# Performance work log

Hardware: AMD Instinct MI355X
Metric: run time of the kernel (lower is better)

Reference implementation:

```python
import jax, jax.numpy as jnp
import numpy as np

B, S, E = 2, 2048, 2048
H, KV, HD = 16, 4, 128          # attn heads, kv heads, head_dim = E//H
GROUPS = H // KV
I = 8192                        # intermediate_size
EPS = 1e-6
ROPE_THETA = 10000.0
SCALE = HD ** -0.5


def _rope_tables(seq_len, head_dim, dtype=jnp.float32):
    inv_freq = 1.0 / (ROPE_THETA ** (jnp.arange(0, head_dim, 2, dtype=jnp.float32) / head_dim))
    pos = jnp.arange(seq_len, dtype=jnp.float32)
    ang = pos[:, None] * inv_freq[None, :]            # [S, HD/2]
    emb = jnp.concatenate([ang, ang], axis=-1)        # [S, HD]
    return jnp.cos(emb).astype(dtype), jnp.sin(emb).astype(dtype)


def _rotate_half(x):
    x1, x2 = jnp.split(x, 2, axis=-1)
    return jnp.concatenate([-x2, x1], axis=-1)


def _apply_rope(x, cos, sin):
    # x: [B, h, S, HD]; cos/sin: [S, HD]
    return x * cos[None, None] + _rotate_half(x) * sin[None, None]


def _rmsnorm(x, w, eps=EPS):
    var = jnp.mean(jnp.square(x), axis=-1, keepdims=True)
    return x * jax.lax.rsqrt(var + eps) * w


def setup_inputs() -> dict:
    key = jax.random.key(0)
    ks = jax.random.split(key, 12)
    sd = lambda fan_in: 1.0 / np.sqrt(fan_in)
    inp = {
        "x": jax.random.normal(ks[0], (B, S, E), dtype=jnp.float32),
        "attn_mask": jnp.zeros((B, 1, S, S), dtype=jnp.bool_),
        "wq": jax.random.normal(ks[1], (E, E), dtype=jnp.float32) * sd(E),
        "bq": jnp.zeros((E,), dtype=jnp.float32),
        "wkv": jax.random.normal(ks[2], (2 * KV * HD, E), dtype=jnp.float32) * sd(E),
        "bkv": jnp.zeros((2 * KV * HD,), dtype=jnp.float32),
        "wo": jax.random.normal(ks[3], (E, E), dtype=jnp.float32) * sd(E),
        "w_gate": jax.random.normal(ks[4], (I, E), dtype=jnp.float32) * sd(E),
        "w_up": jax.random.normal(ks[5], (I, E), dtype=jnp.float32) * sd(E),
        "w_down": jax.random.normal(ks[6], (E, I), dtype=jnp.float32) * sd(I),
        "norm1_w": jnp.ones((E,), dtype=jnp.float32),
        "norm2_w": jnp.ones((E,), dtype=jnp.float32),
    }
    return inp


def reference(x, attn_mask, wq, bq, wkv, bkv, wo, w_gate, w_up, w_down, norm1_w, norm2_w):
    # ---- attention block ----
    y = _rmsnorm(x, norm1_w)
    q = y @ wq.T + bq                                     # [B,S,E]
    kv = y @ wkv.T + bkv                                  # [B,S,2*KV*HD]
    k, v = jnp.split(kv, 2, axis=-1)
    q = q.reshape(B, S, H, HD).transpose(0, 2, 1, 3)      # [B,H,S,HD]
    k = k.reshape(B, S, KV, HD).transpose(0, 2, 1, 3)     # [B,KV,S,HD]
    v = v.reshape(B, S, KV, HD).transpose(0, 2, 1, 3)
    cos, sin = _rope_tables(S, HD, dtype=q.dtype)
    q = _apply_rope(q, cos, sin)
    k = _apply_rope(k, cos, sin)
    # GQA expand kv heads
    k = jnp.repeat(k, GROUPS, axis=1)                     # [B,H,S,HD]
    v = jnp.repeat(v, GROUPS, axis=1)
    # NOTE: source Qwen2Attention.forward never applies attn_mask — faithful here.
    scores = jnp.einsum('bhsd,bhtd->bhst', q, k) * SCALE  # [B,H,S,S]
    attn = jax.nn.softmax(scores, axis=-1)
    o = jnp.einsum('bhst,bhtd->bhsd', attn, v)            # [B,H,S,HD]
    o = o.transpose(0, 2, 1, 3).reshape(B, S, E) @ wo.T
    x = x + o
    # ---- MLP block (SwiGLU) ----
    y = _rmsnorm(x, norm2_w)
    h = jax.nn.silu(y @ w_gate.T) * (y @ w_up.T)          # [B,S,I]
    x = x + h @ w_down.T
    return x
```

## Files before the change

kernel.cpp:

```cpp
#include <hip/hip_runtime.h>

typedef __bf16 bf16;
typedef __bf16 bf16x8 __attribute__((ext_vector_type(8)));
typedef __bf16 bf16x4 __attribute__((ext_vector_type(4)));
typedef float f32x4 __attribute__((ext_vector_type(4)));

#define DEV __device__ __forceinline__

constexpr int B_ = 2, S_ = 2048, E_ = 2048, H_ = 16, KVH_ = 4, HD_ = 128, I_ = 8192;
constexpr int KVROW = 2 * KVH_ * HD_;
constexpr float EPS_ = 1e-6f;
constexpr float SCALE_ = 0.08838834764831845f;

DEV void gload_lds16(const bf16* g, bf16* l) {
  __builtin_amdgcn_global_load_lds(
      (const __attribute__((address_space(1))) void*)g,
      (__attribute__((address_space(3))) void*)l, 16, 0, 0);
}

__global__ __launch_bounds__(256) void cvt6_k(const float* __restrict__ s0, const float* __restrict__ s1,
                                              const float* __restrict__ s2, const float* __restrict__ s3,
                                              const float* __restrict__ s4, const float* __restrict__ s5,
                                              bf16* __restrict__ dst) {
  constexpr size_t N0 = 4194304, N1 = 2097152, N2 = 4194304,
                   N3 = 16777216, N4 = 16777216, N5 = 16777216;
  constexpr size_t TOT = N0 + N1 + N2 + N3 + N4 + N5;
  for (size_t i = ((size_t)blockIdx.x * 256 + threadIdx.x) * 8; i < TOT;
       i += (size_t)gridDim.x * 256 * 8) {
    size_t off = i; const float* sp;
    if (off < N0) sp = s0;
    else if ((off -= N0) < N1) sp = s1;
    else if ((off -= N1) < N2) sp = s2;
    else if ((off -= N2) < N3) sp = s3;
    else if ((off -= N3) < N4) sp = s4;
    else { off -= N4; sp = s5; }
    const float4* p = (const float4*)(sp + off);
    float4 a = p[0], b = p[1];
    bf16x8 o;
    o[0]=(bf16)a.x; o[1]=(bf16)a.y; o[2]=(bf16)a.z; o[3]=(bf16)a.w;
    o[4]=(bf16)b.x; o[5]=(bf16)b.y; o[6]=(bf16)b.z; o[7]=(bf16)b.w;
    *(bf16x8*)(dst + i) = o;
  }
}

template <typename InT>
__global__ __launch_bounds__(256) void rmsnorm_k(const InT* __restrict__ x,
                                                 const float* __restrict__ w,
                                                 bf16* __restrict__ y) {
  const int row = blockIdx.x, t = threadIdx.x;
  const size_t base = (size_t)row * E_ + t * 8;
  float v[8];
  if constexpr (sizeof(InT) == 2) {
    bf16x8 d = *(const bf16x8*)(x + base);
#pragma unroll
    for (int j = 0; j < 8; ++j) v[j] = (float)d[j];
  } else {
    const float4* p = (const float4*)(x + base);
    float4 a = p[0], b2 = p[1];
    v[0]=a.x; v[1]=a.y; v[2]=a.z; v[3]=a.w; v[4]=b2.x; v[5]=b2.y; v[6]=b2.z; v[7]=b2.w;
  }
  float ss = 0.f;
#pragma unroll
  for (int j = 0; j < 8; ++j) ss += v[j] * v[j];
#pragma unroll
  for (int off = 32; off; off >>= 1) ss += __shfl_xor(ss, off);
  __shared__ float red[4];
  if ((t & 63) == 0) red[t >> 6] = ss;
  __syncthreads();
  ss = red[0] + red[1] + red[2] + red[3];
  const float sc = rsqrtf(ss * (1.0f / E_) + EPS_);
  const float4* wp = (const float4*)(w + t * 8);
  float4 wa = wp[0], wb = wp[1];
  float wv[8] = {wa.x, wa.y, wa.z, wa.w, wb.x, wb.y, wb.z, wb.w};
  bf16x8 o;
#pragma unroll
  for (int j = 0; j < 8; ++j) o[j] = (bf16)(v[j] * sc * wv[j]);
  *(bf16x8*)(y + base) = o;
}

__global__ __launch_bounds__(256) void rope_k(bf16* __restrict__ q, bf16* __restrict__ kvb) {
  const int gid = blockIdx.x * 256 + threadIdx.x;
  const int d = gid & 63;
  const int r = gid >> 6;
  const int hh = r % (H_ + KVH_);
  const int s = (r / (H_ + KVH_)) % S_;
  const int b = r / ((H_ + KVH_) * S_);
  bf16* p = (hh < H_) ? (q + (size_t)(b * S_ + s) * E_ + hh * HD_)
                      : (kvb + (size_t)(b * S_ + s) * KVROW + (hh - H_) * HD_);
  const float invf = exp2f(-(float)d * (13.287712379549449f / 64.f));
  float sn, cs;
  sincosf((float)s * invf, &sn, &cs);
  const float x1 = (float)p[d], x2 = (float)p[d + 64];
  p[d] = (bf16)(x1 * cs - x2 * sn);
  p[d + 64] = (bf16)(x2 * cs + x1 * sn);
}

__global__ __launch_bounds__(256) void vtrans_k(const bf16* __restrict__ kvb,
                                                bf16* __restrict__ vT) {
  __shared__ bf16 lds[64 * 136];
  const int t = threadIdx.x;
  const int s0 = blockIdx.x * 64, kvh = blockIdx.y, b = blockIdx.z;
#pragma unroll
  for (int i = 0; i < 4; ++i) {
    const int c = t + i * 256;
    const int row = c >> 4, slot = c & 15;
    *(bf16x8*)&lds[row * 136 + slot * 8] =
        *(const bf16x8*)(kvb + (size_t)(b * S_ + s0 + row) * KVROW + KVH_ * HD_ + kvh * HD_ + slot * 8);
  }
  __syncthreads();
#pragma unroll
  for (int i = 0; i < 4; ++i) {
    const int c = t + i * 256;
    const int d = c >> 3, ss = c & 7;
    bf16x8 pk;
#pragma unroll
    for (int j = 0; j < 8; ++j) pk[j] = lds[(ss * 8 + j) * 136 + d];
    *(bf16x8*)(vT + (size_t)((b * KVH_ + kvh) * HD_ + d) * S_ + s0 + ss * 8) = pk;
  }
}

__global__ __launch_bounds__(256, 2) void gemm_gu(const bf16* __restrict__ A,
                                                  const bf16* __restrict__ Wg,
                                                  const bf16* __restrict__ Wu,
                                                  bf16* __restrict__ out,
                                                  int M, int N, int K) {
  constexpr int BK = 64;
  __shared__ bf16 As[128 * BK];
  __shared__ bf16 Bg[128 * BK];
  __shared__ bf16 Bu[128 * BK];
  const int t = threadIdx.x, lane = t & 63, w = t >> 6;
  const int g = lane >> 4, l15 = lane & 15;
  const int bm = blockIdx.y, bn = blockIdx.x;
  const int wm = w >> 1, wn = w & 1;
  f32x4 ag[4][4], au[4][4];
#pragma unroll
  for (int i = 0; i < 4; ++i)
#pragma unroll
    for (int j = 0; j < 4; ++j) { ag[i][j] = {0.f,0.f,0.f,0.f}; au[i][j] = {0.f,0.f,0.f,0.f}; }

  const bf16* Ab  = A  + (size_t)bm * 128 * K;
  const bf16* Wgb = Wg + (size_t)bn * 128 * K;
  const bf16* Wub = Wu + (size_t)bn * 128 * K;

  for (int k0 = 0; k0 < K; k0 += BK) {
    __syncthreads();
#pragma unroll
    for (int i = 0; i < 4; ++i) {
      const int c = t + i * 256;
      const int row = c >> 3, slot = c & 7;
      const size_t goff = (size_t)row * K + k0 + ((slot ^ (row & 7)) << 3);
      gload_lds16(Ab + goff, &As[c * 8]);
      gload_lds16(Wgb + goff, &Bg[c * 8]);
      gload_lds16(Wub + goff, &Bu[c * 8]);
    }
    __syncthreads();
#pragma unroll
    for (int ks = 0; ks < 2; ++ks) {
      bf16x8 af[4], bgv[4], buv[4];
#pragma unroll
      for (int mt = 0; mt < 4; ++mt) {
        const int row = wm * 64 + mt * 16 + l15;
        af[mt] = *(const bf16x8*)&As[row * BK + (((ks * 4 + g) ^ (row & 7)) << 3)];
      }
#pragma unroll
      for (int nt = 0; nt < 4; ++nt) {
        const int row = wn * 64 + nt * 16 + l15;
        const int off = row * BK + (((ks * 4 + g) ^ (row & 7)) << 3);
        bgv[nt] = *(const bf16x8*)&Bg[off];
        buv[nt] = *(const bf16x8*)&Bu[off];
      }
#pragma unroll
      for (int mt = 0; mt < 4; ++mt)
#pragma unroll
        for (int nt = 0; nt < 4; ++nt) {
          ag[mt][nt] = __builtin_amdgcn_mfma_f32_16x16x32_bf16(af[mt], bgv[nt], ag[mt][nt], 0, 0, 0);
          au[mt][nt] = __builtin_amdgcn_mfma_f32_16x16x32_bf16(af[mt], buv[nt], au[mt][nt], 0, 0, 0);
        }
    }
  }

  const int row0 = bm * 128 + wm * 64;
  const int col0 = bn * 128 + wn * 64;
#pragma unroll
  for (int nt = 0; nt < 4; ++nt) {
    const int col = col0 + nt * 16 + l15;
#pragma unroll
    for (int mt = 0; mt < 4; ++mt) {
#pragma unroll
      for (int r = 0; r < 4; ++r) {
        const int rowi = row0 + mt * 16 + g * 4 + r;
        const float gv = ag[mt][nt][r];
        const float hv = (gv / (1.f + __expf(-gv))) * au[mt][nt][r];
        out[(size_t)rowi * N + col] = (bf16)hv;
      }
    }
  }
}

template <int EPI, bool WB>
__global__ __launch_bounds__(256, 2) void gemm_bt(const bf16* __restrict__ A,
                                                  const void* __restrict__ Wp,
                                                  const float* __restrict__ bias,
                                                  const void* __restrict__ ext,
                                                  void* __restrict__ out,
                                                  int M, int N, int K) {
  constexpr int BK = 64;
  __shared__ bf16 As[128 * BK];
  __shared__ bf16 Bs[128 * BK];
  const int t = threadIdx.x, lane = t & 63, w = t >> 6;
  const int g = lane >> 4, l15 = lane & 15;
  const int bm = blockIdx.y, bn = blockIdx.x;
  const int wm = w >> 1, wn = w & 1;
  f32x4 acc[4][4];
#pragma unroll
  for (int i = 0; i < 4; ++i)
#pragma unroll
    for (int j = 0; j < 4; ++j) acc[i][j] = {0.f, 0.f, 0.f, 0.f};

  const bf16* Ab = A + (size_t)bm * 128 * K;

  for (int k0 = 0; k0 < K; k0 += BK) {
    __syncthreads();
#pragma unroll
    for (int i = 0; i < 4; ++i) {
      const int c = t + i * 256;
      const int row = c >> 3, slot = c & 7;
      gload_lds16(Ab + (size_t)row * K + k0 + ((slot ^ (row & 7)) << 3), &As[c * 8]);
    }
    if constexpr (WB) {
      const bf16* Wb = (const bf16*)Wp + (size_t)bn * 128 * K;
#pragma unroll
      for (int i = 0; i < 4; ++i) {
        const int c = t + i * 256;
        const int row = c >> 3, slot = c & 7;
        gload_lds16(Wb + (size_t)row * K + k0 + ((slot ^ (row & 7)) << 3), &Bs[c * 8]);
      }
    } else {
      const float* Wb = (const float*)Wp + (size_t)bn * 128 * K;
#pragma unroll
      for (int i = 0; i < 4; ++i) {
        const int c = t + i * 256;
        const int row = c >> 3, slot = c & 7;
        const float4* wp = (const float4*)(Wb + (size_t)row * K + k0 + slot * 8);
        float4 w0 = wp[0], w1 = wp[1];
        bf16x8 pk;
        pk[0] = (bf16)w0.x; pk[1] = (bf16)w0.y; pk[2] = (bf16)w0.z; pk[3] = (bf16)w0.w;
        pk[4] = (bf16)w1.x; pk[5] = (bf16)w1.y; pk[6] = (bf16)w1.z; pk[7] = (bf16)w1.w;
        *(bf16x8*)&Bs[row * BK + ((slot ^ (row & 7)) << 3)] = pk;
      }
    }
    __syncthreads();
#pragma unroll
    for (int ks = 0; ks < 2; ++ks) {
      bf16x8 af[4], bfv[4];
#pragma unroll
      for (int mt = 0; mt < 4; ++mt) {
        const int row = wm * 64 + mt * 16 + l15;
        af[mt] = *(const bf16x8*)&As[row * BK + (((ks * 4 + g) ^ (row & 7)) << 3)];
      }
#pragma unroll
      for (int nt = 0; nt < 4; ++nt) {
        const int row = wn * 64 + nt * 16 + l15;
        bfv[nt] = *(const bf16x8*)&Bs[row * BK + (((ks * 4 + g) ^ (row & 7)) << 3)];
      }
#pragma unroll
      for (int mt = 0; mt < 4; ++mt)
#pragma unroll
        for (int nt = 0; nt < 4; ++nt)
          acc[mt][nt] = __builtin_amdgcn_mfma_f32_16x16x32_bf16(af[mt], bfv[nt], acc[mt][nt], 0, 0, 0);
    }
  }

  const int row0 = bm * 128 + wm * 64;
  const int col0 = bn * 128 + wn * 64;
#pragma unroll
  for (int nt = 0; nt < 4; ++nt) {
    const int col = col0 + nt * 16 + l15;
    const float bv = bias ? bias[col] : 0.f;
#pragma unroll
    for (int mt = 0; mt < 4; ++mt) {
#pragma unroll
      for (int r = 0; r < 4; ++r) {
        const int rowi = row0 + mt * 16 + g * 4 + r;
        const size_t idx = (size_t)rowi * N + col;
        float v = acc[mt][nt][r] + bv;
        if constexpr (EPI == 0) {
          ((bf16*)out)[idx] = (bf16)v;
        } else if constexpr (EPI == 1) {
          v += ((const float*)ext)[idx];
          ((bf16*)out)[idx] = (bf16)v;
        } else if constexpr (EPI == 2) {
          const float gv = (float)((const bf16*)ext)[idx];
          const float sg = gv / (1.f + __expf(-gv));
          ((bf16*)out)[idx] = (bf16)(sg * v);
        } else {
          v += (float)((const bf16*)ext)[idx];
          ((float*)out)[idx] = v;
        }
      }
    }
  }
}

__global__ __launch_bounds__(256, 2) void attn_k(const bf16* __restrict__ qb,
                                                 const bf16* __restrict__ kvb,
                                                 const bf16* __restrict__ vT,
                                                 bf16* __restrict__ ob) {
  __shared__ bf16 Ks[64 * 128];
  __shared__ bf16 Vt[128 * 64];
  __shared__ bf16 Ps[4][32 * 64];
  const int t = threadIdx.x, lane = t & 63, w = t >> 6;
  const int g = lane >> 4, l15 = lane & 15;
  const int b = blockIdx.z, h = blockIdx.y;
  const int kvh = h >> 2;
  const int q0 = blockIdx.x * 128 + w * 32;
  const bf16* vTb = vT + (size_t)(b * KVH_ + kvh) * HD_ * S_;

  bf16x8 qf[2][4];
#pragma unroll
  for (int qt = 0; qt < 2; ++qt)
#pragma unroll
    for (int ks = 0; ks < 4; ++ks)
      qf[qt][ks] = *(const bf16x8*)(qb + (size_t)(b * S_ + q0 + qt * 16 + l15) * E_ + h * HD_ + ks * 32 + g * 8);

  f32x4 o[8][2];
#pragma unroll
  for (int i = 0; i < 8; ++i) { o[i][0] = {0.f,0.f,0.f,0.f}; o[i][1] = {0.f,0.f,0.f,0.f}; }
  float mA[2] = {-1e30f, -1e30f}, lA[2] = {0.f, 0.f};

  for (int s0 = 0; s0 < S_; s0 += 64) {
    __syncthreads();
#pragma unroll
    for (int i = 0; i < 4; ++i) {
      const int c = t + i * 256;
      const int row = c >> 4, slot = c & 15;
      gload_lds16(kvb + (size_t)(b * S_ + s0 + row) * KVROW + kvh * HD_ + ((slot ^ (row & 15)) << 3),
                  &Ks[c * 8]);
    }
#pragma unroll
    for (int i = 0; i < 4; ++i) {
      const int c = t + i * 256;
      const int row = c >> 3, slot = c & 7;
      gload_lds16(vTb + (size_t)row * S_ + s0 + ((slot ^ (row & 7)) << 3), &Vt[c * 8]);
    }
    __syncthreads();

    f32x4 sc[2][4];
#pragma unroll
    for (int qt = 0; qt < 2; ++qt)
#pragma unroll
      for (int c = 0; c < 4; ++c) sc[qt][c] = {0.f,0.f,0.f,0.f};
    __builtin_amdgcn_s_setprio(1);
#pragma unroll
    for (int ks = 0; ks < 4; ++ks) {
      bf16x8 kf[4];
#pragma unroll
      for (int c = 0; c < 4; ++c) {
        const int kv = c * 16 + l15;
        kf[c] = *(const bf16x8*)&Ks[kv * 128 + (((ks * 4 + g) ^ (kv & 15)) << 3)];
      }
#pragma unroll
      for (int c = 0; c < 4; ++c) {
        sc[0][c] = __builtin_amdgcn_mfma_f32_16x16x32_bf16(kf[c], qf[0][ks], sc[0][c], 0, 0, 0);
        sc[1][c] = __builtin_amdgcn_mfma_f32_16x16x32_bf16(kf[c], qf[1][ks], sc[1][c], 0, 0, 0);
      }
    }
    __builtin_amdgcn_s_setprio(0);

    float corr[2];
#pragma unroll
    for (int qt = 0; qt < 2; ++qt) {
      float tm = sc[qt][0][0];
#pragma unroll
      for (int c = 0; c < 4; ++c)
#pragma unroll
        for (int r = 0; r < 4; ++r) tm = fmaxf(tm, sc[qt][c][r]);
      tm = fmaxf(tm, __shfl_xor(tm, 16));
      tm = fmaxf(tm, __shfl_xor(tm, 32));
      const float mn = fmaxf(mA[qt], tm);
      corr[qt] = __expf((mA[qt] - mn) * SCALE_);
      mA[qt] = mn;
      float ps = 0.f;
      const int q = qt * 16 + l15;
#pragma unroll
      for (int c = 0; c < 4; ++c)
#pragma unroll
        for (int r = 0; r < 4; ++r) {
          const float p = __expf((sc[qt][c][r] - mn) * SCALE_);
          ps += p;
          const int kv = c * 16 + g * 4 + r;
          Ps[w][q * 64 + (((kv >> 3) ^ (q & 7)) << 3) + (kv & 7)] = (bf16)p;
        }
      ps += __shfl_xor(ps, 16);
      ps += __shfl_xor(ps, 32);
      lA[qt] = lA[qt] * corr[qt] + ps;
#pragma unroll
      for (int dt = 0; dt < 8; ++dt) o[dt][qt] *= corr[qt];
    }
    asm volatile("s_waitcnt lgkmcnt(0)" ::: "memory");
    __builtin_amdgcn_s_setprio(1);
#pragma unroll
    for (int ks = 0; ks < 2; ++ks) {
      bf16x8 pf[2];
#pragma unroll
      for (int qt = 0; qt < 2; ++qt) {
        const int q = qt * 16 + l15;
        pf[qt] = *(const bf16x8*)&Ps[w][q * 64 + (((ks * 4 + g) ^ (q & 7)) << 3)];
      }
#pragma unroll
      for (int dt = 0; dt < 8; ++dt) {
        const int d = dt * 16 + l15;
        const bf16x8 vf = *(const bf16x8*)&Vt[d * 64 + (((ks * 4 + g) ^ (d & 7)) << 3)];
        o[dt][0] = __builtin_amdgcn_mfma_f32_16x16x32_bf16(vf, pf[0], o[dt][0], 0, 0, 0);
        o[dt][1] = __builtin_amdgcn_mfma_f32_16x16x32_bf16(vf, pf[1], o[dt][1], 0, 0, 0);
      }
    }
    __builtin_amdgcn_s_setprio(0);
  }

  const float inv0 = 1.f / lA[0], inv1 = 1.f / lA[1];
  __syncthreads();
  bf16* bb = (w < 2) ? &Ks[(w & 1) * 4096] : &Vt[(w & 1) * 4096];
#pragma unroll
  for (int dt = 0; dt < 8; ++dt)
#pragma unroll
    for (int qt = 0; qt < 2; ++qt) {
      const float iv = qt ? inv1 : inv0;
      bf16x4 pk;
#pragma unroll
      for (int r = 0; r < 4; ++r) pk[r] = (bf16)(o[dt][qt][r] * iv);
      const int q = qt * 16 + l15;
      const int s16 = (dt * 2 + (g >> 1)) ^ (q & 15);
      *(bf16x4*)&bb[q * 128 + (s16 << 3) + ((g & 1) << 2)] = pk;
    }
  asm volatile("s_waitcnt lgkmcnt(0)" ::: "memory");
#pragma unroll
  for (int it = 0; it < 8; ++it) {
    const int c = lane + it * 64;
    const int q = c >> 4, s16 = c & 15;
    const bf16x8 vv = *(const bf16x8*)&bb[q * 128 + ((s16 ^ (q & 15)) << 3)];
    *(bf16x8*)(ob + (size_t)(b * S_ + q0 + q) * E_ + h * HD_ + s16 * 8) = vv;
  }
}

extern "C" void kernel_launch(void* const* d_in, const int* in_sizes, int n_in,
                              void* d_out, int out_size, void* d_ws, size_t ws_size,
                              hipStream_t stream) {
  const float* x   = (const float*)d_in[0];
  const float* wq  = (const float*)d_in[2];
  const float* bq  = (const float*)d_in[3];
  const float* wkv = (const float*)d_in[4];
  const float* bkv = (const float*)d_in[5];
  const float* wo  = (const float*)d_in[6];
  const float* wg  = (const float*)d_in[7];
  const float* wu  = (const float*)d_in[8];
  const float* wd  = (const float*)d_in[9];
  const float* n1  = (const float*)d_in[10];
  const float* n2  = (const float*)d_in[11];
  float* out = (float*)d_out;
  char* ws = (char*)d_ws;
  bf16* y  = (bf16*)(ws);
  bf16* q  = (bf16*)(ws + (16ull << 20));
  bf16* kv = (bf16*)(ws + (32ull << 20));
  bf16* x1 = (bf16*)(ws + (40ull << 20));
  bf16* gh = (bf16*)(ws + (56ull << 20));
  bf16* vT = gh;
  bf16* o  = y;
  bf16* y2 = y;
  bf16* wqb  = (bf16*)(ws + (120ull << 20));
  bf16* wkvb = (bf16*)(ws + (128ull << 20));
  bf16* wob  = (bf16*)(ws + (132ull << 20));
  bf16* wgb  = (bf16*)(ws + (140ull << 20));
  bf16* wub  = (bf16*)(ws + (172ull << 20));
  bf16* wdb  = (bf16*)(ws + (204ull << 20));
  const int M = B_ * S_;
  const bool tierA = ws_size >= (236ull << 20);

  if (tierA)
    cvt6_k<<<2048, 256, 0, stream>>>(wq, wkv, wo, wg, wu, wd, wqb);

  rmsnorm_k<float><<<M, 256, 0, stream>>>(x, n1, y);
  if (tierA) {
    gemm_bt<0, true><<<dim3(E_ / 128, M / 128), 256, 0, stream>>>(y, wqb, bq, nullptr, q, M, E_, E_);
    gemm_bt<0, true><<<dim3(KVROW / 128, M / 128), 256, 0, stream>>>(y, wkvb, bkv, nullptr, kv, M, KVROW, E_);
  } else {
    gemm_bt<0, false><<<dim3(E_ / 128, M / 128), 256, 0, stream>>>(y, wq, bq, nullptr, q, M, E_, E_);
    gemm_bt<0, false><<<dim3(KVROW / 128, M / 128), 256, 0, stream>>>(y, wkv, bkv, nullptr, kv, M, KVROW, E_);
  }
  rope_k<<<(B_ * S_ * (H_ + KVH_) * 64) / 256, 256, 0, stream>>>(q, kv);
  vtrans_k<<<dim3(S_ / 64, KVH_, B_), 256, 0, stream>>>(kv, vT);
  attn_k<<<dim3(S_ / 128, H_, B_), 256, 0, stream>>>(q, kv, vT, o);
  if (tierA) {
    gemm_bt<1, true><<<dim3(E_ / 128, M / 128), 256, 0, stream>>>(o, wob, nullptr, x, x1, M, E_, E_);
    rmsnorm_k<bf16><<<M, 256, 0, stream>>>(x1, n2, y2);
    gemm_gu<<<dim3(I_ / 128, M / 128), 256, 0, stream>>>(y2, wgb, wub, gh, M, I_, E_);
    gemm_bt<3, true><<<dim3(E_ / 128, M / 128), 256, 0, stream>>>(gh, wdb, nullptr, x1, out, M, E_, I_);
  } else {
    gemm_bt<1, false><<<dim3(E_ / 128, M / 128), 256, 0, stream>>>(o, wo, nullptr, x, x1, M, E_, E_);
    rmsnorm_k<bf16><<<M, 256, 0, stream>>>(x1, n2, y2);
    gemm_bt<0, false><<<dim3(I_ / 128, M / 128), 256, 0, stream>>>(y2, wg, nullptr, nullptr, gh, M, I_, E_);
    gemm_bt<2, false><<<dim3(I_ / 128, M / 128), 256, 0, stream>>>(y2, wu, nullptr, gh, gh, M, I_, E_);
    gemm_bt<3, false><<<dim3(E_ / 128, M / 128), 256, 0, stream>>>(gh, wd, nullptr, x1, out, M, E_, I_);
  }
}
```

Measured before the change: 749.4 us.

## Fuse Q and KV projections into one GEMM and widen N tiles to 256

```diff
diff --git a/kernel.cpp b/kernel.cpp
--- a/kernel.cpp
+++ b/kernel.cpp
@@ -9,6 +9,7 @@
 
 constexpr int B_ = 2, S_ = 2048, E_ = 2048, H_ = 16, KVH_ = 4, HD_ = 128, I_ = 8192;
 constexpr int KVROW = 2 * KVH_ * HD_;
+constexpr int QKS = 3072;
 constexpr float EPS_ = 1e-6f;
 constexpr float SCALE_ = 0.08838834764831845f;
 
@@ -78,15 +79,15 @@
   *(bf16x8*)(y + base) = o;
 }
 
-__global__ __launch_bounds__(256) void rope_k(bf16* __restrict__ q, bf16* __restrict__ kvb) {
+__global__ __launch_bounds__(256) void rope_k(bf16* __restrict__ qkvb) {
   const int gid = blockIdx.x * 256 + threadIdx.x;
   const int d = gid & 63;
   const int r = gid >> 6;
   const int hh = r % (H_ + KVH_);
   const int s = (r / (H_ + KVH_)) % S_;
   const int b = r / ((H_ + KVH_) * S_);
-  bf16* p = (hh < H_) ? (q + (size_t)(b * S_ + s) * E_ + hh * HD_)
-                      : (kvb + (size_t)(b * S_ + s) * KVROW + (hh - H_) * HD_);
+  bf16* p = qkvb + (size_t)(b * S_ + s) * QKS +
+            (hh < H_ ? hh * HD_ : 2048 + (hh - H_) * HD_);
   const float invf = exp2f(-(float)d * (13.287712379549449f / 64.f));
   float sn, cs;
   sincosf((float)s * invf, &sn, &cs);
@@ -95,7 +96,7 @@
   p[d + 64] = (bf16)(x2 * cs + x1 * sn);
 }
 
-__global__ __launch_bounds__(256) void vtrans_k(const bf16* __restrict__ kvb,
+__global__ __launch_bounds__(256) void vtrans_k(const bf16* __restrict__ qkvb,
                                                 bf16* __restrict__ vT) {
   __shared__ bf16 lds[64 * 136];
   const int t = threadIdx.x;
@@ -105,7 +106,7 @@
     const int c = t + i * 256;
     const int row = c >> 4, slot = c & 15;
     *(bf16x8*)&lds[row * 136 + slot * 8] =
-        *(const bf16x8*)(kvb + (size_t)(b * S_ + s0 + row) * KVROW + KVH_ * HD_ + kvh * HD_ + slot * 8);
+        *(const bf16x8*)(qkvb + (size_t)(b * S_ + s0 + row) * QKS + 2560 + kvh * HD_ + slot * 8);
   }
   __syncthreads();
 #pragma unroll
@@ -197,9 +198,97 @@
   }
 }
 
-template <int EPI, bool WB>
+template <int EPI, bool BIAS>
+__global__ __launch_bounds__(256, 2) void gemm_n2(const bf16* __restrict__ A,
+                                                  const bf16* __restrict__ W,
+                                                  const float* __restrict__ bias0,
+                                                  const float* __restrict__ bias1,
+                                                  const void* __restrict__ ext,
+                                                  void* __restrict__ out,
+                                                  int M, int N, int K) {
+  constexpr int BK = 64;
+  __shared__ bf16 As[128 * BK];
+  __shared__ bf16 Bs[256 * BK];
+  const int t = threadIdx.x, lane = t & 63, w = t >> 6;
+  const int g = lane >> 4, l15 = lane & 15;
+  const int bm = blockIdx.y, bn = blockIdx.x;
+  const int wm = w >> 1, wn = w & 1;
+  f32x4 acc[4][8];
+#pragma unroll
+  for (int i = 0; i < 4; ++i)
+#pragma unroll
+    for (int j = 0; j < 8; ++j) acc[i][j] = {0.f, 0.f, 0.f, 0.f};
+
+  const bf16* Ab = A + (size_t)bm * 128 * K;
+  const bf16* Wb = W + (size_t)bn * 256 * K;
+
+  for (int k0 = 0; k0 < K; k0 += BK) {
+    __syncthreads();
+#pragma unroll
+    for (int i = 0; i < 4; ++i) {
+      const int c = t + i * 256;
+      const int row = c >> 3, slot = c & 7;
+      gload_lds16(Ab + (size_t)row * K + k0 + ((slot ^ (row & 7)) << 3), &As[c * 8]);
+    }
+#pragma unroll
+    for (int i = 0; i < 8; ++i) {
+      const int c = t + i * 256;
+      const int row = c >> 3, slot = c & 7;
+      gload_lds16(Wb + (size_t)row * K + k0 + ((slot ^ (row & 7)) << 3), &Bs[c * 8]);
+    }
+    __syncthreads();
+#pragma unroll
+    for (int ks = 0; ks < 2; ++ks) {
+      bf16x8 af[4], bfv[8];
+#pragma unroll
+      for (int mt = 0; mt < 4; ++mt) {
+        const int row = wm * 64 + mt * 16 + l15;
+        af[mt] = *(const bf16x8*)&As[row * BK + (((ks * 4 + g) ^ (row & 7)) << 3)];
+      }
+#pragma unroll
+      for (int nt = 0; nt < 8; ++nt) {
+        const int row = wn * 128 + nt * 16 + l15;
+        bfv[nt] = *(const bf16x8*)&Bs[row * BK + (((ks * 4 + g) ^ (row & 7)) << 3)];
+      }
+#pragma unroll
+      for (int mt = 0; mt < 4; ++mt)
+#pragma unroll
+        for (int nt = 0; nt < 8; ++nt)
+          acc[mt][nt] = __builtin_amdgcn_mfma_f32_16x16x32_bf16(af[mt], bfv[nt], acc[mt][nt], 0, 0, 0);
+    }
+  }
+
+  const int row0 = bm * 128 + wm * 64;
+  const int col0 = bn * 256 + wn * 128;
+#pragma unroll
+  for (int nt = 0; nt < 8; ++nt) {
+    const int col = col0 + nt * 16 + l15;
+    float bv = 0.f;
+    if constexpr (BIAS) bv = (col < 2048) ? bias0[col] : bias1[col - 2048];
+#pragma unroll
+    for (int mt = 0; mt < 4; ++mt) {
+#pragma unroll
+      for (int r = 0; r < 4; ++r) {
+        const int rowi = row0 + mt * 16 + g * 4 + r;
+        const size_t idx = (size_t)rowi * N + col;
+        float v = acc[mt][nt][r] + bv;
+        if constexpr (EPI == 0) {
+          ((bf16*)out)[idx] = (bf16)v;
+        } else if constexpr (EPI == 1) {
+          v += ((const float*)ext)[idx];
+          ((bf16*)out)[idx] = (bf16)v;
+        } else {
+          v += (float)((const bf16*)ext)[idx];
+          ((float*)out)[idx] = v;
+        }
+      }
+    }
+  }
+}
+
+template <int EPI>
 __global__ __launch_bounds__(256, 2) void gemm_bt(const bf16* __restrict__ A,
-                                                  const void* __restrict__ Wp,
+                                                  const float* __restrict__ Wp,
                                                   const float* __restrict__ bias,
                                                   const void* __restrict__ ext,
                                                   void* __restrict__ out,
@@ -218,6 +307,7 @@
     for (int j = 0; j < 4; ++j) acc[i][j] = {0.f, 0.f, 0.f, 0.f};
 
   const bf16* Ab = A + (size_t)bm * 128 * K;
+  const float* Wb = Wp + (size_t)bn * 128 * K;
 
   for (int k0 = 0; k0 < K; k0 += BK) {
     __syncthreads();
@@ -227,27 +317,16 @@
       const int row = c >> 3, slot = c & 7;
       gload_lds16(Ab + (size_t)row * K + k0 + ((slot ^ (row & 7)) << 3), &As[c * 8]);
     }
-    if constexpr (WB) {
-      const bf16* Wb = (const bf16*)Wp + (size_t)bn * 128 * K;
-#pragma unroll
-      for (int i = 0; i < 4; ++i) {
-        const int c = t + i * 256;
-        const int row = c >> 3, slot = c & 7;
-        gload_lds16(Wb + (size_t)row * K + k0 + ((slot ^ (row & 7)) << 3), &Bs[c * 8]);
-      }
-    } else {
-      const float* Wb = (const float*)Wp + (size_t)bn * 128 * K;
-#pragma unroll
-      for (int i = 0; i < 4; ++i) {
-        const int c = t + i * 256;
-        const int row = c >> 3, slot = c & 7;
-        const float4* wp = (const float4*)(Wb + (size_t)row * K + k0 + slot * 8);
-        float4 w0 = wp[0], w1 = wp[1];
-        bf16x8 pk;
-        pk[0] = (bf16)w0.x; pk[1] = (bf16)w0.y; pk[2] = (bf16)w0.z; pk[3] = (bf16)w0.w;
-        pk[4] = (bf16)w1.x; pk[5] = (bf16)w1.y; pk[6] = (bf16)w1.z; pk[7] = (bf16)w1.w;
-        *(bf16x8*)&Bs[row * BK + ((slot ^ (row & 7)) << 3)] = pk;
-      }
+#pragma unroll
+    for (int i = 0; i < 4; ++i) {
+      const int c = t + i * 256;
+      const int row = c >> 3, slot = c & 7;
+      const float4* wp = (const float4*)(Wb + (size_t)row * K + k0 + slot * 8);
+      float4 w0 = wp[0], w1 = wp[1];
+      bf16x8 pk;
+      pk[0] = (bf16)w0.x; pk[1] = (bf16)w0.y; pk[2] = (bf16)w0.z; pk[3] = (bf16)w0.w;
+      pk[4] = (bf16)w1.x; pk[5] = (bf16)w1.y; pk[6] = (bf16)w1.z; pk[7] = (bf16)w1.w;
+      *(bf16x8*)&Bs[row * BK + ((slot ^ (row & 7)) << 3)] = pk;
     }
     __syncthreads();
 #pragma unroll
@@ -302,8 +381,7 @@
   }
 }
 
-__global__ __launch_bounds__(256, 2) void attn_k(const bf16* __restrict__ qb,
-                                                 const bf16* __restrict__ kvb,
+__global__ __launch_bounds__(256, 2) void attn_k(const bf16* __restrict__ qkvb,
                                                  const bf16* __restrict__ vT,
                                                  bf16* __restrict__ ob) {
   __shared__ bf16 Ks[64 * 128];
@@ -321,7 +399,7 @@
   for (int qt = 0; qt < 2; ++qt)
 #pragma unroll
     for (int ks = 0; ks < 4; ++ks)
-      qf[qt][ks] = *(const bf16x8*)(qb + (size_t)(b * S_ + q0 + qt * 16 + l15) * E_ + h * HD_ + ks * 32 + g * 8);
+      qf[qt][ks] = *(const bf16x8*)(qkvb + (size_t)(b * S_ + q0 + qt * 16 + l15) * QKS + h * HD_ + ks * 32 + g * 8);
 
   f32x4 o[8][2];
 #pragma unroll
@@ -334,7 +412,7 @@
     for (int i = 0; i < 4; ++i) {
       const int c = t + i * 256;
       const int row = c >> 4, slot = c & 15;
-      gload_lds16(kvb + (size_t)(b * S_ + s0 + row) * KVROW + kvh * HD_ + ((slot ^ (row & 15)) << 3),
+      gload_lds16(qkvb + (size_t)(b * S_ + s0 + row) * QKS + 2048 + kvh * HD_ + ((slot ^ (row & 15)) << 3),
                   &Ks[c * 8]);
     }
 #pragma unroll
@@ -459,47 +537,47 @@
   const float* n2  = (const float*)d_in[11];
   float* out = (float*)d_out;
   char* ws = (char*)d_ws;
-  bf16* y  = (bf16*)(ws);
-  bf16* q  = (bf16*)(ws + (16ull << 20));
-  bf16* kv = (bf16*)(ws + (32ull << 20));
-  bf16* x1 = (bf16*)(ws + (40ull << 20));
-  bf16* gh = (bf16*)(ws + (56ull << 20));
-  bf16* vT = gh;
-  bf16* o  = y;
-  bf16* y2 = y;
-  bf16* wqb  = (bf16*)(ws + (120ull << 20));
-  bf16* wkvb = (bf16*)(ws + (128ull << 20));
-  bf16* wob  = (bf16*)(ws + (132ull << 20));
-  bf16* wgb  = (bf16*)(ws + (140ull << 20));
-  bf16* wub  = (bf16*)(ws + (172ull << 20));
-  bf16* wdb  = (bf16*)(ws + (204ull << 20));
+  bf16* y    = (bf16*)(ws);
+  bf16* qkvb = (bf16*)(ws + (16ull << 20));
+  bf16* x1   = (bf16*)(ws + (40ull << 20));
+  bf16* gh   = (bf16*)(ws + (56ull << 20));
+  bf16* vT   = gh;
+  bf16* o    = y;
+  bf16* y2   = y;
+  bf16* wqkvb = (bf16*)(ws + (120ull << 20));
+  bf16* wob   = (bf16*)(ws + (132ull << 20));
+  bf16* wgb   = (bf16*)(ws + (140ull << 20));
+  bf16* wub   = (bf16*)(ws + (172ull << 20));
+  bf16* wdb   = (bf16*)(ws + (204ull << 20));
   const int M = B_ * S_;
   const bool tierA = ws_size >= (236ull << 20);
 
   if (tierA)
-    cvt6_k<<<2048, 256, 0, stream>>>(wq, wkv, wo, wg, wu, wd, wqb);
+    cvt6_k<<<2048, 256, 0, stream>>>(wq, wkv, wo, wg, wu, wd, wqkvb);
 
   rmsnorm_k<float><<<M, 256, 0, stream>>>(x, n1, y);
   if (tierA) {
-    gemm_bt<0, true><<<dim3(E_ / 128, M / 128), 256, 0, stream>>>(y, wqb, bq, nullptr, q, M, E_, E_);
-    gemm_bt<0, true><<<dim3(KVROW / 128, M / 128), 256, 0, stream>>>(y, wkvb, bkv, nullptr, kv, M, KVROW, E_);
+    gemm_n2<0, true><<<dim3(QKS / 256, M / 128), 256, 0, stream>>>(
+        y, wqkvb, bq, bkv, nullptr, qkvb, M, QKS, E_);
   } else {
-    gemm_bt<0, false><<<dim3(E_ / 128, M / 128), 256, 0, stream>>>(y, wq, bq, nullptr, q, M, E_, E_);
-    gemm_bt<0, false><<<dim3(KVROW / 128, M / 128), 256, 0, stream>>>(y, wkv, bkv, nullptr, kv, M, KVROW, E_);
-  }
-  rope_k<<<(B_ * S_ * (H_ + KVH_) * 64) / 256, 256, 0, stream>>>(q, kv);
-  vtrans_k<<<dim3(S_ / 64, KVH_, B_), 256, 0, stream>>>(kv, vT);
-  attn_k<<<dim3(S_ / 128, H_, B_), 256, 0, stream>>>(q, kv, vT, o);
+    gemm_bt<0><<<dim3(E_ / 128, M / 128), 256, 0, stream>>>(y, wq, bq, nullptr, qkvb, M, QKS, E_);
+    gemm_bt<0><<<dim3(KVROW / 128, M / 128), 256, 0, stream>>>(y, wkv, bkv, nullptr, qkvb + 2048, M, QKS, E_);
+  }
+  rope_k<<<(B_ * S_ * (H_ + KVH_) * 64) / 256, 256, 0, stream>>>(qkvb);
+  vtrans_k<<<dim3(S_ / 64, KVH_, B_), 256, 0, stream>>>(qkvb, vT);
+  attn_k<<<dim3(S_ / 128, H_, B_), 256, 0, stream>>>(qkvb, vT, o);
   if (tierA) {
-    gemm_bt<1, true><<<dim3(E_ / 128, M / 128), 256, 0, stream>>>(o, wob, nullptr, x, x1, M, E_, E_);
+    gemm_n2<1, false><<<dim3(E_ / 256, M / 128), 256, 0, stream>>>(
+        o, wob, nullptr, nullptr, x, x1, M, E_, E_);
     rmsnorm_k<bf16><<<M, 256, 0, stream>>>(x1, n2, y2);
     gemm_gu<<<dim3(I_ / 128, M / 128), 256, 0, stream>>>(y2, wgb, wub, gh, M, I_, E_);
-    gemm_bt<3, true><<<dim3(E_ / 128, M / 128), 256, 0, stream>>>(gh, wdb, nullptr, x1, out, M, E_, I_);
+    gemm_n2<3, false><<<dim3(E_ / 256, M / 128), 256, 0, stream>>>(
+        gh, wdb, nullptr, nullptr, x1, out, M, E_, I_);
   } else {
-    gemm_bt<1, false><<<dim3(E_ / 128, M / 128), 256, 0, stream>>>(o, wo, nullptr, x, x1, M, E_, E_);
+    gemm_bt<1><<<dim3(E_ / 128, M / 128), 256, 0, stream>>>(o, wo, nullptr, x, x1, M, E_, E_);
     rmsnorm_k<bf16><<<M, 256, 0, stream>>>(x1, n2, y2);
-    gemm_bt<0, false><<<dim3(I_ / 128, M / 128), 256, 0, stream>>>(y2, wg, nullptr, nullptr, gh, M, I_, E_);
-    gemm_bt<2, false><<<dim3(I_ / 128, M / 128), 256, 0, stream>>>(y2, wu, nullptr, gh, gh, M, I_, E_);
-    gemm_bt<3, false><<<dim3(E_ / 128, M / 128), 256, 0, stream>>>(gh, wd, nullptr, x1, out, M, E_, I_);
-  }
-}
+    gemm_bt<0><<<dim3(I_ / 128, M / 128), 256, 0, stream>>>(y2, wg, nullptr, nullptr, gh, M, I_, E_);
+    gemm_bt<2><<<dim3(I_ / 128, M / 128), 256, 0, stream>>>(y2, wu, nullptr, gh, gh, M, I_, E_);
+    gemm_bt<3><<<dim3(E_ / 128, M / 128), 256, 0, stream>>>(gh, wd, nullptr, x1, out, M, E_, I_);
+  }
+}
```

Result: slower. 800.3 us (+6.8%).
